# Performance work log

Measured on AMD Instinct MI355X. Metric: run time of the kernel, lower is better.

## Reference

```python
import jax, jax.numpy as jnp
import numpy as np


def _local_indices(H, W, K):
    # KxK local window per pixel; border neighbors clamped to the image (replicate padding)
    half = K // 2
    d = np.arange(-half, half + 1)
    r = np.clip(np.arange(H)[:, None, None, None] + d[None, None, :, None], 0, H - 1)
    c = np.clip(np.arange(W)[None, :, None, None] + d[None, None, None, :], 0, W - 1)
    return (r * W + c).reshape(H * W, K * K).astype(np.int32)


def setup_inputs():
    B, C, H, W = 2, 32, 128, 128
    K, S = 25, 1024
    N = H * W
    k1, k2, k3, k4 = jax.random.split(jax.random.key(0), 4)
    key_feat = jax.random.normal(k1, (B, C, H, W), dtype=jnp.float32)
    query_feat = jax.random.normal(k2, (B, C, H, W), dtype=jnp.float32)
    segment_target = jax.random.randint(k3, (B, 1, H, W), 0, 64, dtype=jnp.int32)
    local = jnp.broadcast_to(jnp.asarray(_local_indices(H, W, K))[None], (B, N, K * K))
    rand_glob = jax.random.randint(k4, (B, N, S - K * K), 0, N, dtype=jnp.int32)
    sample_inds = jnp.concatenate([local, rand_glob], axis=-1)  # [B, N, S]
    return {"key_feat": key_feat, "query_feat": query_feat,
            "segment_target": segment_target, "sample_inds": sample_inds}


def _affinity_logits(key_f, query_f, sample_inds, chunk=1024):
    # key_f, query_f: [B, N, C]; sample_inds: [B, N, S]
    B, N, C = key_f.shape
    S = sample_inds.shape[-1]
    nchunks = N // chunk
    q_c = query_f.reshape(B, nchunks, chunk, C).transpose(1, 0, 2, 3)
    i_c = sample_inds.reshape(B, nchunks, chunk, S).transpose(1, 0, 2, 3)

    def body(carry, args):
        q, idx = args                                   # [B, chunk, C], [B, chunk, S]
        kg = jax.vmap(lambda kb, ib: kb[ib])(key_f, idx)  # [B, chunk, S, C]
        return carry, jnp.einsum('bnsc,bnc->bns', kg, q)

    _, lc = jax.lax.scan(body, None, (q_c, i_c))        # [nchunks, B, chunk, S]
    logits = lc.transpose(1, 0, 2, 3).reshape(B, N, S)
    return logits * (C ** -0.5)


def _loss(logits, sample_inds, segment_target):
    B, N, S = logits.shape
    seg = segment_target.reshape(B, N)
    samples = jax.vmap(lambda s, i: s[i])(seg, sample_inds)      # [B, N, S]
    targets = (seg[:, :, None] == samples).astype(logits.dtype)
    mask = (seg != 0).astype(logits.dtype)[:, :, None]           # [B, N, 1]
    # weighted_softmax(logits, mask)
    xe = jnp.exp(logits - jnp.max(logits, -1, keepdims=True))
    denom = jnp.sum(xe * mask, -1, keepdims=True)
    y_prob = xe * mask / (denom + 1e-9)
    y_pred = jnp.log(jnp.clip(y_prob, 1e-8, None))
    y_true = targets / (jnp.sum(targets, -1, keepdims=True) + 1e-9)
    # F.kl_div(y_pred, y_true, reduction='none') with 0*log(0) = 0
    kl = jnp.where(y_true > 0,
                   y_true * (jnp.log(jnp.clip(y_true, 1e-30, None)) - y_pred),
                   0.0) * mask
    agg_mask = (jnp.sum(mask, -1) > 0).astype(logits.dtype)
    return jnp.sum(kl) / (jnp.sum(agg_mask) + 1e-9)


def reference(key_feat, query_feat, segment_target, sample_inds):
    B, C, H, W = key_feat.shape
    N = H * W
    key_f = key_feat.reshape(B, C, N).transpose(0, 2, 1)    # [B, N, C]
    query_f = query_feat.reshape(B, C, N).transpose(0, 2, 1)
    logits = _affinity_logits(key_f, query_f, sample_inds)  # [B, N, S], scaled by C**-0.5
    loss = _loss(logits, sample_inds, segment_target)
    return (logits, loss)
```

## Files before the change

### kernel.cpp

```cpp
#include <hip/hip_runtime.h>
#include <stdint.h>

typedef _Float16 h2 __attribute__((ext_vector_type(2)));
typedef _Float16 h4 __attribute__((ext_vector_type(4)));
typedef float    f4 __attribute__((ext_vector_type(4)));

static constexpr int CDIM = 32;
static constexpr int NPIX = 16384;
static constexpr int SSAM = 1024;
static constexpr int NLOC = 625;
static constexpr int NRND = SSAM - NLOC;
static constexpr int ROWS_PER_BLOCK = 16;

__device__ __forceinline__ uint16_t f2h(float f) {
    union { _Float16 h; uint16_t u; } c;
    c.h = (_Float16)f;
    return c.u;
}

template<int CTRL>
__device__ __forceinline__ float dpp_add(float x) {
    int y = __builtin_amdgcn_mov_dpp(__float_as_int(x), CTRL, 0xF, 0xF, true);
    return x + __int_as_float(y);
}

__device__ __forceinline__ float dot2(h2 a, h2 b, float c) {
    return __builtin_amdgcn_fdot2(a, b, c, false);
}

__global__ __launch_bounds__(256)
void prep_kernel(const float* __restrict__ key_f,
                 const float* __restrict__ query_f,
                 const int* __restrict__ seg32,
                 uint8_t* __restrict__ key16,
                 uint8_t* __restrict__ q16,
                 uint8_t* __restrict__ seg8,
                 uint32_t* __restrict__ segbit,
                 int N, int rows, float scale)
{
    int gI = blockIdx.x * 256 + threadIdx.x;
    if (gI >= rows) return;
    segbit[2 * gI]     = 0;
    segbit[2 * gI + 1] = 0;
    seg8[gI] = (uint8_t)seg32[gI];

    int b = gI / N, n = gI - b * N;
    const size_t cb = (size_t)b * CDIM;

    uint32_t kp[16], qp[16];
#pragma unroll
    for (int c = 0; c < CDIM; c += 2) {
        float k0 = key_f[(cb + c) * N + n];
        float k1 = key_f[(cb + c + 1) * N + n];
        float q0 = query_f[(cb + c) * N + n] * scale;
        float q1 = query_f[(cb + c + 1) * N + n] * scale;
        kp[c >> 1] = (uint32_t)f2h(k0) | ((uint32_t)f2h(k1) << 16);
        qp[c >> 1] = (uint32_t)f2h(q0) | ((uint32_t)f2h(q1) << 16);
    }
    uint4* ko = (uint4*)(key16 + ((size_t)gI << 6));
    uint4* qo = (uint4*)(q16 + ((size_t)gI << 6));
#pragma unroll
    for (int j = 0; j < 4; ++j) {
        ko[j] = make_uint4(kp[4*j], kp[4*j+1], kp[4*j+2], kp[4*j+3]);
        qo[j] = make_uint4(qp[4*j], qp[4*j+1], qp[4*j+2], qp[4*j+3]);
    }
}

__global__ __launch_bounds__(256)
void segbit_build(const int* __restrict__ seg32,
                  uint32_t* __restrict__ segbit,
                  int N, int rows)
{
    int g = blockIdx.x * 256 + threadIdx.x;
    if (g >= rows) return;
    int b = g / N, n = g - b * N;
    int v = seg32[g] & 63;
    atomicOr(&segbit[(((size_t)(b * 64 + v)) << 9) + (n >> 5)], 1u << (n & 31));
}

__global__ __launch_bounds__(256)
void dense_local(const uint8_t* __restrict__ key16,
                 const uint8_t* __restrict__ q16,
                 const uint8_t* __restrict__ seg8,
                 float* __restrict__ out,
                 float* __restrict__ zA,
                 float* __restrict__ tA,
                 float* __restrict__ slA)
{
    const int tid  = threadIdx.x;
    const int bid  = blockIdx.x;
    const int b    = bid >> 8;
    const int t8   = bid & 255;
    const int y0   = (t8 >> 4) << 3;
    const int x0   = (t8 & 15) << 3;
    const int lane = tid & 63;
    const int w    = tid >> 6;

    __shared__ __align__(16) uint8_t  kslot[256 * 80];
    __shared__ __align__(16) _Float16 res[4][16][256];
    __shared__ uint8_t wseg[1024];
    __shared__ float   rowacc[4][16][3];

    const uint8_t* kb = key16 + ((size_t)b << 20);
    const uint8_t* sb = seg8 + ((size_t)b << 14);
    const int yo = y0 - 12, xo = x0 - 12;

    for (int s = tid; s < 1024; s += 256) {
        int i = s >> 5, j = s & 31;
        int yy = min(max(yo + i, 0), 127);
        int xx = min(max(xo + j, 0), 127);
        wseg[s] = sb[(yy << 7) + xx];
    }
    if (tid < 192) ((float*)rowacc)[tid] = 0.f;

    const int qsel = (w << 4) + (lane & 15);
    const int qyA  = qsel >> 3, qxA = qsel & 7;
    const size_t qrow = ((size_t)b << 14) + ((size_t)(y0 + qyA) << 7) + (x0 + qxA);
    const int koff = (lane >> 4) << 3;
    const h4 a0 = *(const h4*)(q16 + (qrow << 6) + koff);
    const h4 a1 = *(const h4*)(q16 + (qrow << 6) + 32 + koff);

    __syncthreads();

    for (int t = 0; t < 4; ++t) {
        for (int s = tid; s < 1024; s += 256) {
            int slot = s >> 2, q = s & 3;
            int i = (t << 3) + (slot >> 5), j = slot & 31;
            int yy = min(max(yo + i, 0), 127);
            int xx = min(max(xo + j, 0), 127);
            *(uint4*)(kslot + slot * 80 + (q << 4)) =
                *(const uint4*)(kb + ((((size_t)(yy << 7)) + xx) << 6) + (q << 4));
        }
        __syncthreads();

#pragma unroll 4
        for (int n = 0; n < 16; ++n) {
            const uint8_t* kr = kslot + ((n << 4) + (lane & 15)) * 80;
            h4 b0 = *(const h4*)(kr + koff);
            h4 b1 = *(const h4*)(kr + 32 + koff);
            f4 acc = {0.f, 0.f, 0.f, 0.f};
            acc = __builtin_amdgcn_mfma_f32_16x16x16f16(a0, b0, acc, 0, 0, 0);
            acc = __builtin_amdgcn_mfma_f32_16x16x16f16(a1, b1, acc, 0, 0, 0);
#pragma unroll
            for (int r = 0; r < 4; ++r)
                res[w][((lane >> 4) << 2) + r][(n << 4) + (lane & 15)] =
                    (_Float16)acc[r];
        }

        for (int m = 0; m < 16; ++m) {
            const int q  = (w << 4) + m;
            const int qy = q >> 3, qx = q & 7;
            const int row = (b << 14) + ((y0 + qy) << 7) + (x0 + qx);
            const int segr = (int)wseg[((qy + 12) << 5) + qx + 12];
            int sLo = ((t << 3) - qy) * 25; if (sLo < 0) sLo = 0;
            int sHi = ((t << 3) - qy + 8) * 25; if (sHi > NLOC) sHi = NLOC;
            float z = 0.f, tc = 0.f, sl = 0.f;
            for (int s = sLo + lane; s < sHi; s += 64) {
                int d25 = (s * 5243) >> 17;
                int r25 = s - d25 * 25;
                int i  = qy + d25;
                int wc = qx + r25;
                float v = (float)res[w][m][((i - (t << 3)) << 5) + wc];
                out[((size_t)row << 10) + s] = v;
                z += __expf(v);
                if ((int)wseg[(i << 5) + wc] == segr) { tc += 1.f; sl += v; }
            }
#pragma unroll
            for (int off = 32; off >= 1; off >>= 1) {
                z  += __shfl_xor(z,  off, 64);
                tc += __shfl_xor(tc, off, 64);
                sl += __shfl_xor(sl, off, 64);
            }
            if (lane == 0) {
                rowacc[w][m][0] += z;
                rowacc[w][m][1] += tc;
                rowacc[w][m][2] += sl;
            }
        }
        __syncthreads();
    }

    if (tid < 64) {
        int q = tid, qy = q >> 3, qx = q & 7;
        int row = (b << 14) + ((y0 + qy) << 7) + (x0 + qx);
        zA[row]  = rowacc[q >> 4][q & 15][0];
        tA[row]  = rowacc[q >> 4][q & 15][1];
        slA[row] = rowacc[q >> 4][q & 15][2];
    }
}

__global__ __launch_bounds__(256)
void affinity_rand(const int* __restrict__ inds,
                   const uint8_t* __restrict__ key16,
                   const uint8_t* __restrict__ q16,
                   const int* __restrict__ seg32,
                   const uint32_t* __restrict__ segbit,
                   const float* __restrict__ zA,
                   const float* __restrict__ tA,
                   const float* __restrict__ slA,
                   float* __restrict__ out,
                   float* __restrict__ ws_kl)
{
    const int tid  = threadIdx.x;
    const int row0 = blockIdx.x * ROWS_PER_BLOCK;
    const int b    = row0 >> 14;
    const int lane = tid & 63;
    const int w    = tid >> 6;
    const int g    = lane >> 2;
    const int sub  = lane & 3;
    const int gidx = (w << 4) + g;
    const int half = tid >> 7;
    const int ht   = tid & 127;

    __shared__ __align__(16) int      idx_lds[2][2][448];
    __shared__ __align__(16) uint32_t bm_lds[2][2][512];
    __shared__ float red[2][6][4];
    __shared__ float zp[ROWS_PER_BLOCK], tp[ROWS_PER_BLOCK], sp[ROWS_PER_BLOCK];

    const uint32_t* sbm = segbit + ((size_t)(b * 64) << 9);

    if (tid < ROWS_PER_BLOCK)             zp[tid] = zA[row0 + tid];
    else if (tid < 2*ROWS_PER_BLOCK)      tp[tid - ROWS_PER_BLOCK] = tA[row0 + tid - ROWS_PER_BLOCK];
    else if (tid < 3*ROWS_PER_BLOCK)      sp[tid - 2*ROWS_PER_BLOCK] = slA[row0 + tid - 2*ROWS_PER_BLOCK];

    {
        const int* ib = inds + ((size_t)(row0 + half) << 10) + NLOC;
        idx_lds[0][half][ht]       = ib[ht];
        idx_lds[0][half][ht + 128] = ib[ht + 128];
        idx_lds[0][half][ht + 256] = ib[ht + 256];
        if (ht < NRND - 384)
            idx_lds[0][half][ht + 384] = ib[ht + 384];
        int sh = seg32[row0 + half];
        ((uint4*)bm_lds[0][half])[ht] =
            ((const uint4*)(sbm + ((size_t)(sh & 63) << 9)))[ht];
    }
    int scurA = seg32[row0];
    int scurB = seg32[row0 + 1];
    uint4 qcurA = *(const uint4*)(q16 + ((size_t)row0 << 6) + (sub << 4));
    uint4 qcurB = *(const uint4*)(q16 + ((size_t)(row0 + 1) << 6) + (sub << 4));
    __syncthreads();

    const uint8_t* kp = key16 + ((size_t)b << 20);
    const uint32_t subs = (uint32_t)(sub << 4);
    const bool act6 = (384 + gidx) < NRND;
    const bool owned1 = (sub < 2) || (sub == 2 && act6);

    for (int t = 0; t < ROWS_PER_BLOCK / 2; ++t) {
        const int rowA = row0 + 2 * t;
        const int rowB = rowA + 1;
        const int pp   = t & 1;
        const int* curA = idx_lds[pp][0];
        const int* curB = idx_lds[pp][1];
        const bool hasNext = (t + 1 < ROWS_PER_BLOCK / 2);

        h2 qa0, qa1, qa2, qa3, qb0, qb1, qb2, qb3;
        {
            union { uint4 u; h2 h[4]; } qc;
            qc.u = qcurA; qa0 = qc.h[0]; qa1 = qc.h[1]; qa2 = qc.h[2]; qa3 = qc.h[3];
            qc.u = qcurB; qb0 = qc.h[0]; qb1 = qc.h[1]; qb2 = qc.h[2]; qb3 = qc.h[3];
        }
        const int segA = scurA, segB = scurB;

        int ixA[7], ixB[7];
#pragma unroll
        for (int i = 0; i < 7; ++i) {
            ixA[i] = curA[(i << 6) + gidx];
            ixB[i] = curB[(i << 6) + gidx];
        }

        uint4 ka[7], kb_[7];
#pragma unroll
        for (int i = 0; i < 6; ++i) {
            ka[i]  = *(const uint4*)(kp + (((uint32_t)ixA[i] << 6) | subs));
            kb_[i] = *(const uint4*)(kp + (((uint32_t)ixB[i] << 6) | subs));
        }
        ka[6] = make_uint4(0, 0, 0, 0);
        kb_[6] = make_uint4(0, 0, 0, 0);
        if (act6) {
            ka[6]  = *(const uint4*)(kp + (((uint32_t)ixA[6] << 6) | subs));
            kb_[6] = *(const uint4*)(kp + (((uint32_t)ixB[6] << 6) | subs));
        }

        int pf0 = 0, pf1 = 0, pf2 = 0, pf3 = 0;
        uint4 bmn; int snA = 0, snB = 0;
        uint4 qnA, qnB;
        if (hasNext) {
            const int* ibn = inds + ((size_t)(rowA + 2 + half) << 10) + NLOC;
            pf0 = ibn[ht];
            pf1 = ibn[ht + 128];
            pf2 = ibn[ht + 256];
            if (ht < NRND - 384) pf3 = ibn[ht + 384];
            snA = seg32[rowA + 2];
            snB = seg32[rowA + 3];
            int sh = half ? snB : snA;
            bmn = ((const uint4*)(sbm + ((size_t)(sh & 63) << 9)))[ht];
            qnA = *(const uint4*)(q16 + ((size_t)(rowA + 2) << 6) + (sub << 4));
            qnB = *(const uint4*)(q16 + ((size_t)(rowA + 3) << 6) + (sub << 4));
        }
        int tfmA = 0, tfmB = 0;
        {
            int i0 = curA[(sub << 6) + gidx];
            if ((bm_lds[pp][0][i0 >> 5] >> (i0 & 31)) & 1u) tfmA |= 1;
            int i1 = curB[(sub << 6) + gidx];
            if ((bm_lds[pp][1][i1 >> 5] >> (i1 & 31)) & 1u) tfmB |= 1;
            if (sub < 3) {
                int j0 = curA[((sub + 4) << 6) + gidx];
                if (owned1 && ((bm_lds[pp][0][j0 >> 5] >> (j0 & 31)) & 1u)) tfmA |= 2;
                int j1 = curB[((sub + 4) << 6) + gidx];
                if (owned1 && ((bm_lds[pp][1][j1 >> 5] >> (j1 & 31)) & 1u)) tfmB |= 2;
            }
        }

        const size_t obA = ((size_t)rowA << 10) + NLOC;
        const size_t obB = ((size_t)rowB << 10) + NLOC;
        float lgA0 = 0.f, lgA1 = 0.f, lgB0 = 0.f, lgB1 = 0.f;
#pragma unroll
        for (int it = 0; it < 7; ++it) {
            union { uint4 u; h2 h[4]; } kc;
            kc.u = ka[it];
            float aA = dot2(kc.h[0], qa0, 0.f);
            aA = dot2(kc.h[1], qa1, aA);
            aA = dot2(kc.h[2], qa2, aA);
            aA = dot2(kc.h[3], qa3, aA);
            kc.u = kb_[it];
            float aB = dot2(kc.h[0], qb0, 0.f);
            aB = dot2(kc.h[1], qb1, aB);
            aB = dot2(kc.h[2], qb2, aB);
            aB = dot2(kc.h[3], qb3, aB);
            aA = dpp_add<0xB1>(aA); aA = dpp_add<0x4E>(aA);
            aB = dpp_add<0xB1>(aB); aB = dpp_add<0x4E>(aB);
            if (sub == (it & 3)) {
                if (it < 4) { lgA0 = aA; lgB0 = aB; }
                else        { lgA1 = aA; lgB1 = aB; }
                if (it < 6 || act6) {
                    out[obA + (it << 6) + gidx] = aA;
                    out[obB + (it << 6) + gidx] = aB;
                }
            }
        }

        float z0 = __expf(lgA0) + (owned1 ? __expf(lgA1) : 0.f);
        float z1 = __expf(lgB0) + (owned1 ? __expf(lgB1) : 0.f);
        float c0 = (float)__popc((unsigned)tfmA);
        float c1 = (float)__popc((unsigned)tfmB);
        float s0 = ((tfmA & 1) ? lgA0 : 0.f) + ((tfmA & 2) ? lgA1 : 0.f);
        float s1 = ((tfmB & 1) ? lgB0 : 0.f) + ((tfmB & 2) ? lgB1 : 0.f);
#pragma unroll
        for (int off = 32; off >= 1; off >>= 1) {
            z0 += __shfl_xor(z0, off, 64);
            z1 += __shfl_xor(z1, off, 64);
            c0 += __shfl_xor(c0, off, 64);
            c1 += __shfl_xor(c1, off, 64);
            s0 += __shfl_xor(s0, off, 64);
            s1 += __shfl_xor(s1, off, 64);
        }
        if (lane == 0) {
            red[pp][0][w] = z0; red[pp][1][w] = c0; red[pp][2][w] = s0;
            red[pp][3][w] = z1; red[pp][4][w] = c1; red[pp][5][w] = s1;
        }

        if (hasNext) {
            idx_lds[pp ^ 1][half][ht]       = pf0;
            idx_lds[pp ^ 1][half][ht + 128] = pf1;
            idx_lds[pp ^ 1][half][ht + 256] = pf2;
            if (ht < NRND - 384) idx_lds[pp ^ 1][half][ht + 384] = pf3;
            ((uint4*)bm_lds[pp ^ 1][half])[ht] = bmn;
            qcurA = qnA; qcurB = qnB;
            scurA = snA; scurB = snB;
        }
        __syncthreads();

        if (tid < 2) {
            const int  row  = rowA + tid;
            const int  sgn  = tid ? segB : segA;
            const int  base = tid * 3;
            if (sgn != 0) {
                const float Z  = zp[2*t + tid] +
                    (red[pp][base][0] + red[pp][base][1]) + (red[pp][base][2] + red[pp][base][3]);
                const float T  = tp[2*t + tid] +
                    (red[pp][base+1][0] + red[pp][base+1][1]) + (red[pp][base+1][2] + red[pp][base+1][3]);
                const float SL = sp[2*t + tid] +
                    (red[pp][base+2][0] + red[pp][base+2][1]) + (red[pp][base+2][2] + red[pp][base+2][3]);
                ws_kl[row] = -__logf(T) - SL / T + __logf(Z);
            } else {
                ws_kl[row] = 0.f;
            }
        }
    }
}

__global__ __launch_bounds__(256)
void affinity_fallback(const float* __restrict__ key_f,
                       const float* __restrict__ query_f,
                       const int*   __restrict__ seg32,
                       const int*   __restrict__ inds,
                       float* __restrict__ out,
                       float* __restrict__ ws_kl,
                       int N, int S, float scale)
{
    const int bid = blockIdx.x;
    const int tid = threadIdx.x;
    const int b   = bid / N;

    __shared__ float q_lds[CDIM];
    __shared__ float redA[4], redB[4], redC[4];

    if (tid < CDIM) {
        int n = bid - b * N;
        q_lds[tid] = query_f[((size_t)(b * CDIM + tid)) * N + n];
    }
    const int seg_n = seg32[bid];
    __syncthreads();

    float q[CDIM];
#pragma unroll
    for (int c = 0; c < CDIM; ++c) q[c] = q_lds[c];

    const size_t rowbase = (size_t)bid * S;
    const int4 iv = ((const int4*)(inds + rowbase))[tid];
    const int idxv[4] = {iv.x, iv.y, iv.z, iv.w};

    float lg[4];
    int   tf[4];
#pragma unroll
    for (int k = 0; k < 4; ++k) {
        int idx = idxv[k];
        tf[k] = (seg32[b * N + idx] == seg_n) ? 1 : 0;
        float acc = 0.f;
#pragma unroll
        for (int c = 0; c < CDIM; ++c)
            acc = fmaf(key_f[((size_t)(b * CDIM + c)) * N + idx], q[c], acc);
        lg[k] = acc * scale;
    }
    ((float4*)(out + rowbase))[tid] = make_float4(lg[0], lg[1], lg[2], lg[3]);

    const int lane = tid & 63, wv = tid >> 6;
    float m = fmaxf(fmaxf(lg[0], lg[1]), fmaxf(lg[2], lg[3]));
#pragma unroll
    for (int off = 32; off >= 1; off >>= 1)
        m = fmaxf(m, __shfl_xor(m, off, 64));
    if (lane == 0) redA[wv] = m;
    __syncthreads();
    m = fmaxf(fmaxf(redA[0], redA[1]), fmaxf(redA[2], redA[3]));

    float e[4], z = 0.f, tcnt = 0.f;
#pragma unroll
    for (int k = 0; k < 4; ++k) {
        e[k] = expf(lg[k] - m);
        z += e[k];
        tcnt += (float)tf[k];
    }
#pragma unroll
    for (int off = 32; off >= 1; off >>= 1) {
        z    += __shfl_xor(z, off, 64);
        tcnt += __shfl_xor(tcnt, off, 64);
    }
    if (lane == 0) { redB[wv] = z; redC[wv] = tcnt; }
    __syncthreads();
    const float Z = redB[0] + redB[1] + redB[2] + redB[3];
    const float T = redC[0] + redC[1] + redC[2] + redC[3];

    float kl = 0.f;
    if (seg_n != 0) {
        const float invZ = 1.f / (Z + 1e-9f);
        const float invT = 1.f / (T + 1e-9f);
        const float nlT  = -logf(T + 1e-9f);
#pragma unroll
        for (int k = 0; k < 4; ++k) {
            if (tf[k]) {
                float p = e[k] * invZ;
                float yp = logf(fmaxf(p, 1e-8f));
                kl += invT * (nlT - yp);
            }
        }
    }
#pragma unroll
    for (int off = 32; off >= 1; off >>= 1)
        kl += __shfl_xor(kl, off, 64);
    if (lane == 0) redA[wv] = kl;
    __syncthreads();
    if (tid == 0)
        ws_kl[bid] = redA[0] + redA[1] + redA[2] + redA[3];
}

__global__ __launch_bounds__(1024)
void loss_reduce(const float* __restrict__ ws_kl,
                 const int* __restrict__ seg32,
                 float* __restrict__ out_loss, int rows)
{
    const int tid = threadIdx.x;
    float s = 0.f, c = 0.f;
    for (int i = tid; i < rows; i += 1024) {
        s += ws_kl[i];
        c += (seg32[i] != 0) ? 1.f : 0.f;
    }
#pragma unroll
    for (int off = 32; off >= 1; off >>= 1) {
        s += __shfl_xor(s, off, 64);
        c += __shfl_xor(c, off, 64);
    }
    __shared__ float sA[16], sB[16];
    const int lane = tid & 63, wv = tid >> 6;
    if (lane == 0) { sA[wv] = s; sB[wv] = c; }
    __syncthreads();
    if (tid == 0) {
        float ts = 0.f, tc = 0.f;
#pragma unroll
        for (int k = 0; k < 16; ++k) { ts += sA[k]; tc += sB[k]; }
        out_loss[0] = ts / (tc + 1e-9f);
    }
}

extern "C" void kernel_launch(void* const* d_in, const int* in_sizes, int n_in,
                              void* d_out, int out_size, void* d_ws, size_t ws_size,
                              hipStream_t stream)
{
    const float* key_f   = (const float*)d_in[0];
    const float* query_f = (const float*)d_in[1];
    const int*   seg32   = (const int*)d_in[2];
    const int*   inds    = (const int*)d_in[3];
    float* out = (float*)d_out;

    const int N    = NPIX;
    const int rows = in_sizes[2];
    const int S    = in_sizes[3] / rows;
    const float scale = (float)(1.0 / sqrt((double)CDIM));
    const int B    = rows / N;

    const size_t off_q16 = (size_t)rows * 64;
    const size_t off_s8  = off_q16 + (size_t)rows * 64;
    const size_t off_sb  = (off_s8 + (size_t)rows + 255) & ~(size_t)255;
    const size_t sb_words = (size_t)B * 64 * 512;
    const size_t off_zA  = (off_sb + sb_words * 4 + 255) & ~(size_t)255;
    const size_t off_tA  = off_zA + (size_t)rows * 4;
    const size_t off_slA = off_tA + (size_t)rows * 4;
    const size_t off_kl  = off_slA + (size_t)rows * 4;
    const size_t need    = off_kl + (size_t)rows * 4;

    uint8_t* wsb = (uint8_t*)d_ws;
    const bool geom_ok = (S == SSAM) && (rows % N == 0) &&
                         (rows % ROWS_PER_BLOCK == 0);

    if (ws_size >= need && geom_ok) {
        uint8_t*  key16  = wsb;
        uint8_t*  q16    = wsb + off_q16;
        uint8_t*  seg8   = wsb + off_s8;
        uint32_t* segbit = (uint32_t*)(wsb + off_sb);
        float*    zA     = (float*)(wsb + off_zA);
        float*    tA     = (float*)(wsb + off_tA);
        float*    slA    = (float*)(wsb + off_slA);
        float*    wskl   = (float*)(wsb + off_kl);

        prep_kernel<<<(rows + 255) / 256, 256, 0, stream>>>(
            key_f, query_f, seg32, key16, q16, seg8, segbit, N, rows, scale);
        segbit_build<<<(rows + 255) / 256, 256, 0, stream>>>(
            seg32, segbit, N, rows);
        dense_local<<<B * 256, 256, 0, stream>>>(
            key16, q16, seg8, out, zA, tA, slA);
        affinity_rand<<<rows / ROWS_PER_BLOCK, 256, 0, stream>>>(
            inds, key16, q16, seg32, segbit, zA, tA, slA, out, wskl);
        loss_reduce<<<1, 1024, 0, stream>>>(wskl, seg32, out + (size_t)rows * S, rows);
    } else {
        float* wskl = (float*)d_ws;
        affinity_fallback<<<rows, 256, 0, stream>>>(
            key_f, query_f, seg32, inds, out, wskl, N, S, scale);
        loss_reduce<<<1, 1024, 0, stream>>>(wskl, seg32, out + (size_t)rows * S, rows);
    }
}
```

Baseline: 165.5 us.

## Fuse dense-local and random-sample affinity kernels into one launch with shared LDS

```diff
diff --git a/kernel.cpp b/kernel.cpp
--- a/kernel.cpp
+++ b/kernel.cpp
@@ -11,6 +11,8 @@
 static constexpr int NLOC = 625;
 static constexpr int NRND = SSAM - NLOC;
 static constexpr int ROWS_PER_BLOCK = 16;
+
+static constexpr int SMEM_BYTES = 28416;
 
 __device__ __forceinline__ uint16_t f2h(float f) {
     union { _Float16 h; uint16_t u; } c;
@@ -78,17 +80,17 @@
     atomicOr(&segbit[(((size_t)(b * 64 + v)) << 9) + (n >> 5)], 1u << (n & 31));
 }
 
-__global__ __launch_bounds__(256)
-void dense_local(const uint8_t* __restrict__ key16,
-                 const uint8_t* __restrict__ q16,
-                 const uint8_t* __restrict__ seg8,
-                 float* __restrict__ out,
-                 float* __restrict__ zA,
-                 float* __restrict__ tA,
-                 float* __restrict__ slA)
+__device__ __forceinline__
+void dense_path(uint8_t* smem, int bid,
+                const uint8_t* __restrict__ key16,
+                const uint8_t* __restrict__ q16,
+                const uint8_t* __restrict__ seg8,
+                float* __restrict__ out,
+                float* __restrict__ zA,
+                float* __restrict__ tA,
+                float* __restrict__ slA)
 {
     const int tid  = threadIdx.x;
-    const int bid  = blockIdx.x;
     const int b    = bid >> 8;
     const int t8   = bid & 255;
     const int y0   = (t8 >> 4) << 3;
@@ -96,10 +98,10 @@
     const int lane = tid & 63;
     const int w    = tid >> 6;
 
-    __shared__ __align__(16) uint8_t  kslot[256 * 80];
-    __shared__ __align__(16) _Float16 res[4][16][256];
-    __shared__ uint8_t wseg[1024];
-    __shared__ float   rowacc[4][16][3];
+    uint8_t*  kslot  = smem;
+    _Float16* res    = (_Float16*)(smem + 10240);
+    uint8_t*  wseg   = smem + 26624;
+    float*    rowacc = (float*)(smem + 27648);
 
     const uint8_t* kb = key16 + ((size_t)b << 20);
     const uint8_t* sb = seg8 + ((size_t)b << 14);
@@ -111,7 +113,7 @@
         int xx = min(max(xo + j, 0), 127);
         wseg[s] = sb[(yy << 7) + xx];
     }
-    if (tid < 192) ((float*)rowacc)[tid] = 0.f;
+    if (tid < 192) rowacc[tid] = 0.f;
 
     const int qsel = (w << 4) + (lane & 15);
     const int qyA  = qsel >> 3, qxA = qsel & 7;
@@ -122,10 +124,10 @@
 
     __syncthreads();
 
-    for (int t = 0; t < 4; ++t) {
-        for (int s = tid; s < 1024; s += 256) {
+    for (int t = 0; t < 8; ++t) {
+        for (int s = tid; s < 512; s += 256) {
             int slot = s >> 2, q = s & 3;
-            int i = (t << 3) + (slot >> 5), j = slot & 31;
+            int i = (t << 2) + (slot >> 5), j = slot & 31;
             int yy = min(max(yo + i, 0), 127);
             int xx = min(max(xo + j, 0), 127);
             *(uint4*)(kslot + slot * 80 + (q << 4)) =
@@ -133,8 +135,8 @@
         }
         __syncthreads();
 
-#pragma unroll 4
-        for (int n = 0; n < 16; ++n) {
+#pragma unroll
+        for (int n = 0; n < 8; ++n) {
             const uint8_t* kr = kslot + ((n << 4) + (lane & 15)) * 80;
             h4 b0 = *(const h4*)(kr + koff);
             h4 b1 = *(const h4*)(kr + 32 + koff);
@@ -142,9 +144,11 @@
             acc = __builtin_amdgcn_mfma_f32_16x16x16f16(a0, b0, acc, 0, 0, 0);
             acc = __builtin_amdgcn_mfma_f32_16x16x16f16(a1, b1, acc, 0, 0, 0);
 #pragma unroll
-            for (int r = 0; r < 4; ++r)
-                res[w][((lane >> 4) << 2) + r][(n << 4) + (lane & 15)] =
+            for (int r = 0; r < 4; ++r) {
+                int m = ((lane >> 4) << 2) + r;
+                res[(w * 16 + m) * 128 + (n << 4) + (lane & 15)] =
                     (_Float16)acc[r];
+            }
         }
 
         for (int m = 0; m < 16; ++m) {
@@ -152,15 +156,16 @@
             const int qy = q >> 3, qx = q & 7;
             const int row = (b << 14) + ((y0 + qy) << 7) + (x0 + qx);
             const int segr = (int)wseg[((qy + 12) << 5) + qx + 12];
-            int sLo = ((t << 3) - qy) * 25; if (sLo < 0) sLo = 0;
-            int sHi = ((t << 3) - qy + 8) * 25; if (sHi > NLOC) sHi = NLOC;
+            int sLo = ((t << 2) - qy) * 25; if (sLo < 0) sLo = 0;
+            int sHi = ((t << 2) - qy + 4) * 25; if (sHi > NLOC) sHi = NLOC;
             float z = 0.f, tc = 0.f, sl = 0.f;
             for (int s = sLo + lane; s < sHi; s += 64) {
                 int d25 = (s * 5243) >> 17;
                 int r25 = s - d25 * 25;
                 int i  = qy + d25;
                 int wc = qx + r25;
-                float v = (float)res[w][m][((i - (t << 3)) << 5) + wc];
+                float v = (float)res[(w * 16 + m) * 128 +
+                                     (((i - (t << 2)) << 5) + wc)];
                 out[((size_t)row << 10) + s] = v;
                 z += __expf(v);
                 if ((int)wseg[(i << 5) + wc] == segr) { tc += 1.f; sl += v; }
@@ -172,9 +177,9 @@
                 sl += __shfl_xor(sl, off, 64);
             }
             if (lane == 0) {
-                rowacc[w][m][0] += z;
-                rowacc[w][m][1] += tc;
-                rowacc[w][m][2] += sl;
+                rowacc[(w * 16 + m) * 3 + 0] += z;
+                rowacc[(w * 16 + m) * 3 + 1] += tc;
+                rowacc[(w * 16 + m) * 3 + 2] += sl;
             }
         }
         __syncthreads();
@@ -183,26 +188,26 @@
     if (tid < 64) {
         int q = tid, qy = q >> 3, qx = q & 7;
         int row = (b << 14) + ((y0 + qy) << 7) + (x0 + qx);
-        zA[row]  = rowacc[q >> 4][q & 15][0];
-        tA[row]  = rowacc[q >> 4][q & 15][1];
-        slA[row] = rowacc[q >> 4][q & 15][2];
-    }
-}
-
-__global__ __launch_bounds__(256)
-void affinity_rand(const int* __restrict__ inds,
-                   const uint8_t* __restrict__ key16,
-                   const uint8_t* __restrict__ q16,
-                   const int* __restrict__ seg32,
-                   const uint32_t* __restrict__ segbit,
-                   const float* __restrict__ zA,
-                   const float* __restrict__ tA,
-                   const float* __restrict__ slA,
-                   float* __restrict__ out,
-                   float* __restrict__ ws_kl)
+        zA[row]  = rowacc[q * 3 + 0];
+        tA[row]  = rowacc[q * 3 + 1];
+        slA[row] = rowacc[q * 3 + 2];
+    }
+}
+
+__device__ __forceinline__
+void rand_path(uint8_t* smem, int rbid,
+               const int* __restrict__ inds,
+               const uint8_t* __restrict__ key16,
+               const uint8_t* __restrict__ q16,
+               const int* __restrict__ seg32,
+               const uint32_t* __restrict__ segbit,
+               float* __restrict__ out,
+               float* __restrict__ zB,
+               float* __restrict__ tB,
+               float* __restrict__ slB)
 {
     const int tid  = threadIdx.x;
-    const int row0 = blockIdx.x * ROWS_PER_BLOCK;
+    const int row0 = rbid * ROWS_PER_BLOCK;
     const int b    = row0 >> 14;
     const int lane = tid & 63;
     const int w    = tid >> 6;
@@ -212,26 +217,21 @@
     const int half = tid >> 7;
     const int ht   = tid & 127;
 
-    __shared__ __align__(16) int      idx_lds[2][2][448];
-    __shared__ __align__(16) uint32_t bm_lds[2][2][512];
-    __shared__ float red[2][6][4];
-    __shared__ float zp[ROWS_PER_BLOCK], tp[ROWS_PER_BLOCK], sp[ROWS_PER_BLOCK];
+    int*      idxp = (int*)smem;
+    uint32_t* bmp  = (uint32_t*)(smem + 7168);
+    float*    redp = (float*)(smem + 15360);
 
     const uint32_t* sbm = segbit + ((size_t)(b * 64) << 9);
-
-    if (tid < ROWS_PER_BLOCK)             zp[tid] = zA[row0 + tid];
-    else if (tid < 2*ROWS_PER_BLOCK)      tp[tid - ROWS_PER_BLOCK] = tA[row0 + tid - ROWS_PER_BLOCK];
-    else if (tid < 3*ROWS_PER_BLOCK)      sp[tid - 2*ROWS_PER_BLOCK] = slA[row0 + tid - 2*ROWS_PER_BLOCK];
 
     {
         const int* ib = inds + ((size_t)(row0 + half) << 10) + NLOC;
-        idx_lds[0][half][ht]       = ib[ht];
-        idx_lds[0][half][ht + 128] = ib[ht + 128];
-        idx_lds[0][half][ht + 256] = ib[ht + 256];
-        if (ht < NRND - 384)
-            idx_lds[0][half][ht + 384] = ib[ht + 384];
+        int* d = idxp + half * 448;
+        d[ht]       = ib[ht];
+        d[ht + 128] = ib[ht + 128];
+        d[ht + 256] = ib[ht + 256];
+        if (ht < NRND - 384) d[ht + 384] = ib[ht + 384];
         int sh = seg32[row0 + half];
-        ((uint4*)bm_lds[0][half])[ht] =
+        ((uint4*)(bmp + half * 512))[ht] =
             ((const uint4*)(sbm + ((size_t)(sh & 63) << 9)))[ht];
     }
     int scurA = seg32[row0];
@@ -249,8 +249,10 @@
         const int rowA = row0 + 2 * t;
         const int rowB = rowA + 1;
         const int pp   = t & 1;
-        const int* curA = idx_lds[pp][0];
-        const int* curB = idx_lds[pp][1];
+        const int* curA = idxp + (pp * 2 + 0) * 448;
+        const int* curB = idxp + (pp * 2 + 1) * 448;
+        const uint32_t* bmA = bmp + (pp * 2 + 0) * 512;
+        const uint32_t* bmB = bmp + (pp * 2 + 1) * 512;
         const bool hasNext = (t + 1 < ROWS_PER_BLOCK / 2);
 
         h2 qa0, qa1, qa2, qa3, qb0, qb1, qb2, qb3;
@@ -259,7 +261,6 @@
             qc.u = qcurA; qa0 = qc.h[0]; qa1 = qc.h[1]; qa2 = qc.h[2]; qa3 = qc.h[3];
             qc.u = qcurB; qb0 = qc.h[0]; qb1 = qc.h[1]; qb2 = qc.h[2]; qb3 = qc.h[3];
         }
-        const int segA = scurA, segB = scurB;
 
         int ixA[7], ixB[7];
 #pragma unroll
@@ -300,14 +301,14 @@
         int tfmA = 0, tfmB = 0;
         {
             int i0 = curA[(sub << 6) + gidx];
-            if ((bm_lds[pp][0][i0 >> 5] >> (i0 & 31)) & 1u) tfmA |= 1;
+            if ((bmA[i0 >> 5] >> (i0 & 31)) & 1u) tfmA |= 1;
             int i1 = curB[(sub << 6) + gidx];
-            if ((bm_lds[pp][1][i1 >> 5] >> (i1 & 31)) & 1u) tfmB |= 1;
+            if ((bmB[i1 >> 5] >> (i1 & 31)) & 1u) tfmB |= 1;
             if (sub < 3) {
                 int j0 = curA[((sub + 4) << 6) + gidx];
-                if (owned1 && ((bm_lds[pp][0][j0 >> 5] >> (j0 & 31)) & 1u)) tfmA |= 2;
+                if (owned1 && ((bmA[j0 >> 5] >> (j0 & 31)) & 1u)) tfmA |= 2;
                 int j1 = curB[((sub + 4) << 6) + gidx];
-                if (owned1 && ((bm_lds[pp][1][j1 >> 5] >> (j1 & 31)) & 1u)) tfmB |= 2;
+                if (owned1 && ((bmB[j1 >> 5] >> (j1 & 31)) & 1u)) tfmB |= 2;
             }
         }
 
@@ -355,37 +356,96 @@
             s1 += __shfl_xor(s1, off, 64);
         }
         if (lane == 0) {
-            red[pp][0][w] = z0; red[pp][1][w] = c0; red[pp][2][w] = s0;
-            red[pp][3][w] = z1; red[pp][4][w] = c1; red[pp][5][w] = s1;
+            redp[(pp * 6 + 0) * 4 + w] = z0;
+            redp[(pp * 6 + 1) * 4 + w] = c0;
+            redp[(pp * 6 + 2) * 4 + w] = s0;
+            redp[(pp * 6 + 3) * 4 + w] = z1;
+            redp[(pp * 6 + 4) * 4 + w] = c1;
+            redp[(pp * 6 + 5) * 4 + w] = s1;
         }
 
         if (hasNext) {
-            idx_lds[pp ^ 1][half][ht]       = pf0;
-            idx_lds[pp ^ 1][half][ht + 128] = pf1;
-            idx_lds[pp ^ 1][half][ht + 256] = pf2;
-            if (ht < NRND - 384) idx_lds[pp ^ 1][half][ht + 384] = pf3;
-            ((uint4*)bm_lds[pp ^ 1][half])[ht] = bmn;
+            int* d = idxp + ((pp ^ 1) * 2 + half) * 448;
+            d[ht]       = pf0;
+            d[ht + 128] = pf1;
+            d[ht + 256] = pf2;
+            if (ht < NRND - 384) d[ht + 384] = pf3;
+            ((uint4*)(bmp + ((pp ^ 1) * 2 + half) * 512))[ht] = bmn;
             qcurA = qnA; qcurB = qnB;
             scurA = snA; scurB = snB;
         }
         __syncthreads();
 
         if (tid < 2) {
-            const int  row  = rowA + tid;
-            const int  sgn  = tid ? segB : segA;
-            const int  base = tid * 3;
-            if (sgn != 0) {
-                const float Z  = zp[2*t + tid] +
-                    (red[pp][base][0] + red[pp][base][1]) + (red[pp][base][2] + red[pp][base][3]);
-                const float T  = tp[2*t + tid] +
-                    (red[pp][base+1][0] + red[pp][base+1][1]) + (red[pp][base+1][2] + red[pp][base+1][3]);
-                const float SL = sp[2*t + tid] +
-                    (red[pp][base+2][0] + red[pp][base+2][1]) + (red[pp][base+2][2] + red[pp][base+2][3]);
-                ws_kl[row] = -__logf(T) - SL / T + __logf(Z);
-            } else {
-                ws_kl[row] = 0.f;
-            }
-        }
+            const int row  = rowA + tid;
+            const int base = pp * 6 + tid * 3;
+            zB[row]  = (redp[(base+0)*4+0] + redp[(base+0)*4+1]) +
+                       (redp[(base+0)*4+2] + redp[(base+0)*4+3]);
+            tB[row]  = (redp[(base+1)*4+0] + redp[(base+1)*4+1]) +
+                       (redp[(base+1)*4+2] + redp[(base+1)*4+3]);
+            slB[row] = (redp[(base+2)*4+0] + redp[(base+2)*4+1]) +
+                       (redp[(base+2)*4+2] + redp[(base+2)*4+3]);
+        }
+    }
+    (void)scurA; (void)scurB;
+}
+
+__global__ __launch_bounds__(256)
+void fused_affinity(const int* __restrict__ inds,
+                    const uint8_t* __restrict__ key16,
+                    const uint8_t* __restrict__ q16,
+                    const uint8_t* __restrict__ seg8,
+                    const int* __restrict__ seg32,
+                    const uint32_t* __restrict__ segbit,
+                    float* __restrict__ out,
+                    float* __restrict__ zA, float* __restrict__ tA,
+                    float* __restrict__ slA,
+                    float* __restrict__ zB, float* __restrict__ tB,
+                    float* __restrict__ slB,
+                    int dense_blocks)
+{
+    __shared__ __align__(16) uint8_t smem[SMEM_BYTES];
+    const int bid = blockIdx.x;
+    if (bid < dense_blocks)
+        dense_path(smem, bid, key16, q16, seg8, out, zA, tA, slA);
+    else
+        rand_path(smem, bid - dense_blocks, inds, key16, q16, seg32, segbit,
+                  out, zB, tB, slB);
+}
+
+__global__ __launch_bounds__(1024)
+void loss_combine(const float* __restrict__ zA, const float* __restrict__ tA,
+                  const float* __restrict__ slA,
+                  const float* __restrict__ zB, const float* __restrict__ tB,
+                  const float* __restrict__ slB,
+                  const int* __restrict__ seg32,
+                  float* __restrict__ out_loss, int rows)
+{
+    const int tid = threadIdx.x;
+    float s = 0.f, c = 0.f;
+    for (int i = tid; i < rows; i += 1024) {
+        if (seg32[i] != 0) {
+            float Z  = zA[i] + zB[i];
+            float T  = tA[i] + tB[i];
+            float SL = slA[i] + slB[i];
+            s += -__logf(T) - SL / T + __logf(Z);
+            c += 1.f;
+        }
+    }
+#pragma unroll
+    for (int off = 32; off >= 1; off >>= 1) {
+        s += __shfl_xor(s, off, 64);
+        c += __shfl_xor(c, off, 64);
+    }
+    __shared__ float sA[16], sB[16];
+    const int lane = tid & 63, wv = tid >> 6;
+    if (lane == 0) { sA[wv] = s; sB[wv] = c; }
+    __syncthreads();
+    if (tid == 0) {
+        float ts = 0.f, tc = 0.f;
+#pragma unroll
+        for (int k = 0; k < 16; ++k) { ts += sA[k]; tc += sB[k]; }
+        out_loss[0] = ts / (tc + 1e-9f);
     }
 }
 
@@ -484,9 +544,9 @@
 }
 
 __global__ __launch_bounds__(1024)
-void loss_reduce(const float* __restrict__ ws_kl,
-                 const int* __restrict__ seg32,
-                 float* __restrict__ out_loss, int rows)
+void loss_reduce_fb(const float* __restrict__ ws_kl,
+                    const int* __restrict__ seg32,
+                    float* __restrict__ out_loss, int rows)
 {
     const int tid = threadIdx.x;
     float s = 0.f, c = 0.f;
@@ -531,11 +591,9 @@
     const size_t off_s8  = off_q16 + (size_t)rows * 64;
     const size_t off_sb  = (off_s8 + (size_t)rows + 255) & ~(size_t)255;
     const size_t sb_words = (size_t)B * 64 * 512;
-    const size_t off_zA  = (off_sb + sb_words * 4 + 255) & ~(size_t)255;
-    const size_t off_tA  = off_zA + (size_t)rows * 4;
-    const size_t off_slA = off_tA + (size_t)rows * 4;
-    const size_t off_kl  = off_slA + (size_t)rows * 4;
-    const size_t need    = off_kl + (size_t)rows * 4;
+    const size_t off_arr = (off_sb + sb_words * 4 + 255) & ~(size_t)255;
+    const size_t arr_sz  = (size_t)rows * 4;
+    const size_t need    = off_arr + arr_sz * 6;
 
     uint8_t* wsb = (uint8_t*)d_ws;
     const bool geom_ok = (S == SSAM) && (rows % N == 0) &&
@@ -546,24 +604,30 @@
         uint8_t*  q16    = wsb + off_q16;
         uint8_t*  seg8   = wsb + off_s8;
         uint32_t* segbit = (uint32_t*)(wsb + off_sb);
-        float*    zA     = (float*)(wsb + off_zA);
-        float*    tA     = (float*)(wsb + off_tA);
-        float*    slA    = (float*)(wsb + off_slA);
-        float*    wskl   = (float*)(wsb + off_kl);
+        float*    zA     = (float*)(wsb + off_arr);
+        float*    tA     = (float*)(wsb + off_arr + arr_sz);
+        float*    slA    = (float*)(wsb + off_arr + arr_sz * 2);
+        float*    zB     = (float*)(wsb + off_arr + arr_sz * 3);
+        float*    tB     = (float*)(wsb + off_arr + arr_sz * 4);
+        float*    slB    = (float*)(wsb + off_arr + arr_sz * 5);
+
+        const int dense_blocks = B * 256;
+        const int rand_blocks  = rows / ROWS_PER_BLOCK;
 
         prep_kernel<<<(rows + 255) / 256, 256, 0, stream>>>(
             key_f, query_f, seg32, key16, q16, seg8, segbit, N, rows, scale);
         segbit_build<<<(rows + 255) / 256, 256, 0, stream>>>(
             seg32, segbit, N, rows);
-        dense_local<<<B * 256, 256, 0, stream>>>(
-            key16, q16, seg8, out, zA, tA, slA);
-        affinity_rand<<<rows / ROWS_PER_BLOCK, 256, 0, stream>>>(
-            inds, key16, q16, seg32, segbit, zA, tA, slA, out, wskl);
-        loss_reduce<<<1, 1024, 0, stream>>>(wskl, seg32, out + (size_t)rows * S, rows);
+        fused_affinity<<<dense_blocks + rand_blocks, 256, 0, stream>>>(
+            inds, key16, q16, seg8, seg32, segbit, out,
+            zA, tA, slA, zB, tB, slB, dense_blocks);
+        loss_combine<<<1, 1024, 0, stream>>>(
+            zA, tA, slA, zB, tB, slB, seg32, out + (size_t)rows * S, rows);
     } else {
         float* wskl = (float*)d_ws;
         affinity_fallback<<<rows, 256, 0, stream>>>(
             key_f, query_f, seg32, inds, out, wskl, N, S, scale);
-        loss_reduce<<<1, 1024, 0, stream>>>(wskl, seg32, out + (size_t)rows * S, rows);
-    }
-}
+        loss_reduce_fb<<<1, 1024, 0, stream>>>(
+            wskl, seg32, out + (size_t)rows * S, rows);
+    }
+}
```

New measurement: 169.0 us (median of 2 runs). +2.1%, slower.
